# Optimization experiments

Measured on AMD Instinct MI355X. Metric: run time of the kernel, lower is better.

## Reference

```python
import jax, jax.numpy as jnp
import numpy as np

BANDWIDTH = 1.0


def setup_inputs() -> dict:
    key = jax.random.key(0)
    k1, k2 = jax.random.split(key)
    test_data = jax.random.normal(k1, (8192, 512), dtype=jnp.float32)
    train_data = jax.random.normal(k2, (16384, 512), dtype=jnp.float32)
    return {"test_data": test_data, "train_data": train_data}


def reference(test_data, train_data):
    # test_data: [N, D], train_data: [M, D]
    bw = jnp.asarray(BANDWIDTH, dtype=test_data.dtype)
    n_train, d = train_data.shape
    # (avoids materializing the [N, M, D] difference tensor)
    x2 = jnp.sum(test_data * test_data, axis=-1, keepdims=True)        # [N, 1]
    y2 = jnp.sum(train_data * train_data, axis=-1)[None, :]           # [1, M]
    xy = jnp.einsum('nd,md->nm', test_data, train_data)               # [N, M]
    sq_dist = jnp.maximum(x2 + y2 - 2.0 * xy, 0.0)                    # [N, M]
    log_exp = -0.5 * sq_dist / (bw * bw)
    # normalization constant z = 0.5*d*log(2*pi) + d*log(bw) + log(n)
    z = (0.5 * d * jnp.log(jnp.asarray(2.0 * np.pi, dtype=test_data.dtype))
         + d * jnp.log(bw)
         + jnp.log(jnp.asarray(float(n_train), dtype=test_data.dtype)))
    return jax.scipy.special.logsumexp(log_exp - z, axis=-1)          # [N]
```

## Files before the change

kernel.cpp:

```cpp
#include <hip/hip_runtime.h>

#define D 512
#define NTEST 8192
#define NTRAIN 16384
#define BN 128
#define BM 128
#define KB 128
#define NCHUNK 8
#define NPART (NCHUNK * 2)
#define CHUNK_M (NTRAIN / NCHUNK)
#define TILES (CHUNK_M / BM)
#define ZCONST 480.20058952863157f

typedef __attribute__((ext_vector_type(4))) int int4v;
typedef __attribute__((ext_vector_type(8))) int int8v;
typedef __attribute__((ext_vector_type(4))) float floatx4;

__device__ __forceinline__ void async_copy16(const void* g, void* l) {
  __builtin_amdgcn_global_load_lds(
      (const __attribute__((address_space(1))) unsigned int*)g,
      (__attribute__((address_space(3))) unsigned int*)l, 16, 0, 0);
}

__global__ __launch_bounds__(256) void prep_kernel(
    const float* __restrict__ test, const float* __restrict__ train,
    unsigned char* __restrict__ testq, unsigned char* __restrict__ trainq,
    float* __restrict__ x2, float* __restrict__ y2) {
  const int gw = (int)((blockIdx.x * blockDim.x + threadIdx.x) >> 6);
  const int lane = threadIdx.x & 63;
  const float* src;
  unsigned char* dst;
  float* sq;
  if (gw < NTEST) {
    src = test + (size_t)gw * D;
    dst = testq + (size_t)gw * D;
    sq = x2 + gw;
  } else {
    const int r = gw - NTEST;
    src = train + (size_t)r * D;
    dst = trainq + (size_t)r * D;
    sq = y2 + r;
  }
  const int kb = lane >> 4;
  const int q = (lane >> 2) & 3;
  const int h = (lane >> 1) & 1;
  const int hb = lane & 1;
  const int sbase = kb * 128 + q * 32 + h * 16 + hb * 8;
  const int dbase = kb * 128 + h * 64 + q * 16 + hb * 8;
  float4 v0 = *(const float4*)(src + sbase);
  float4 v1 = *(const float4*)(src + sbase + 4);
  float s = v0.x * v0.x + v0.y * v0.y + v0.z * v0.z + v0.w * v0.w +
            v1.x * v1.x + v1.y * v1.y + v1.z * v1.z + v1.w * v1.w;
  int w0 = __builtin_amdgcn_cvt_pk_fp8_f32(v0.x, v0.y, 0, false);
  w0 = __builtin_amdgcn_cvt_pk_fp8_f32(v0.z, v0.w, w0, true);
  int w1 = __builtin_amdgcn_cvt_pk_fp8_f32(v1.x, v1.y, 0, false);
  w1 = __builtin_amdgcn_cvt_pk_fp8_f32(v1.z, v1.w, w1, true);
  int2 pv;
  pv.x = w0;
  pv.y = w1;
  *(int2*)(dst + dbase) = pv;
#pragma unroll
  for (int off = 32; off >= 1; off >>= 1) s += __shfl_xor(s, off);
  if (lane == 0) *sq = s;
}

__global__ __launch_bounds__(256, 2) void fused_kernel(
    const unsigned char* __restrict__ A, const unsigned char* __restrict__ B,
    const float* __restrict__ y2, float* __restrict__ part_m,
    float* __restrict__ part_l) {
  __shared__ unsigned char sA0[BN * KB];
  __shared__ unsigned char sA1[BN * KB];
  __shared__ unsigned char sB0[BM * KB];
  __shared__ unsigned char sB1[BM * KB];
  const int tid = threadIdx.x;
  const int lane = tid & 63;
  const int w = tid >> 6;
  const int lm = lane & 15;
  const int lk = lane >> 4;
  const int rowbase = blockIdx.x * BN;
  const int chunk = blockIdx.y;
  const int wrow = (w >> 1) * 64;
  const int wcol = (w & 1) * 64;

  size_t aS[4], bS[4];
  int dO[4];
#pragma unroll
  for (int i = 0; i < 4; ++i) {
    const int o = tid * 16 + i * 4096;
    const int r = o >> 7;
    const int csw = (o >> 4) & 7;
    const int off = ((csw ^ (r & 7)) << 4);
    dO[i] = o;
    aS[i] = (size_t)(rowbase + r) * D + off;
    bS[i] = (size_t)r * D + off;
  }
  int aOffLo[4], aOffHi[4], bOffLo[4], bOffHi[4];
#pragma unroll
  for (int i = 0; i < 4; ++i) {
    const int arow = wrow + i * 16 + lm;
    aOffLo[i] = arow * KB + ((lk ^ (arow & 7)) << 4);
    aOffHi[i] = arow * KB + (((4 + lk) ^ (arow & 7)) << 4);
    const int brow = wcol + i * 16 + lm;
    bOffLo[i] = brow * KB + ((lk ^ (brow & 7)) << 4);
    bOffHi[i] = brow * KB + (((4 + lk) ^ (brow & 7)) << 4);
  }

  auto stage = [&](unsigned char* sa, unsigned char* sb, size_t bcolD,
                   int kb) {
#pragma unroll
    for (int i = 0; i < 4; ++i) {
      async_copy16(A + aS[i] + kb * 128, sa + dO[i]);
      async_copy16(B + bcolD + bS[i] + kb * 128, sb + dO[i]);
    }
  };

  floatx4 acc[4][4];
  auto compute = [&](const unsigned char* sa, const unsigned char* sb) {
    int8v af[4], bf[4];
#pragma unroll
    for (int rt = 0; rt < 4; ++rt) {
      int4v lo = *(const int4v*)&sa[aOffLo[rt]];
      int4v hi = *(const int4v*)&sa[aOffHi[rt]];
      af[rt] = __builtin_shufflevector(lo, hi, 0, 1, 2, 3, 4, 5, 6, 7);
    }
#pragma unroll
    for (int ct = 0; ct < 4; ++ct) {
      int4v lo = *(const int4v*)&sb[bOffLo[ct]];
      int4v hi = *(const int4v*)&sb[bOffHi[ct]];
      bf[ct] = __builtin_shufflevector(lo, hi, 0, 1, 2, 3, 4, 5, 6, 7);
    }
#pragma unroll
    for (int rt = 0; rt < 4; ++rt)
#pragma unroll
      for (int ct = 0; ct < 4; ++ct)
        acc[rt][ct] = __builtin_amdgcn_mfma_scale_f32_16x16x128_f8f6f4(
            af[rt], bf[ct], acc[rt][ct], 0, 0, 0, 127, 0, 127);
  };

  float run_m[16], run_l[16];
#pragma unroll
  for (int i = 0; i < 16; ++i) { run_m[i] = -1e30f; run_l[i] = 0.f; }

  stage(sA0, sB0, (size_t)(chunk * CHUNK_M) * D, 0);
  __syncthreads();

  for (int t = 0; t < TILES; ++t) {
    const int colbase = chunk * CHUNK_M + t * BM;
    const size_t bcolD = (size_t)colbase * D;
    float y2v[4];
#pragma unroll
    for (int ct = 0; ct < 4; ++ct)
      y2v[ct] = y2[colbase + wcol + ct * 16 + lm];

#pragma unroll
    for (int rt = 0; rt < 4; ++rt)
#pragma unroll
      for (int ct = 0; ct < 4; ++ct)
        acc[rt][ct] = floatx4{0.f, 0.f, 0.f, 0.f};

    stage(sA1, sB1, bcolD, 1);
    compute(sA0, sB0);
    __syncthreads();
    stage(sA0, sB0, bcolD, 2);
    compute(sA1, sB1);
    __syncthreads();
    stage(sA1, sB1, bcolD, 3);
    compute(sA0, sB0);
    __syncthreads();
    if (t + 1 < TILES) stage(sA0, sB0, bcolD + (size_t)BM * D, 0);
    compute(sA1, sB1);

#pragma unroll
    for (int rt = 0; rt < 4; ++rt) {
#pragma unroll
      for (int reg = 0; reg < 4; ++reg) {
        const int idx = rt * 4 + reg;
        const float v0 = fmaf(-0.5f, y2v[0], acc[rt][0][reg]);
        const float v1 = fmaf(-0.5f, y2v[1], acc[rt][1][reg]);
        const float v2 = fmaf(-0.5f, y2v[2], acc[rt][2][reg]);
        const float v3 = fmaf(-0.5f, y2v[3], acc[rt][3][reg]);
        const float tmax = fmaxf(fmaxf(v0, v1), fmaxf(v2, v3));
        const float nm = fmaxf(run_m[idx], tmax);
        const float alpha = __expf(run_m[idx] - nm);
        const float ps = __expf(v0 - nm) + __expf(v1 - nm) +
                         __expf(v2 - nm) + __expf(v3 - nm);
        run_l[idx] = fmaf(run_l[idx], alpha, ps);
        run_m[idx] = nm;
      }
    }
    __syncthreads();
  }

  const int slot = chunk * 2 + (w & 1);
#pragma unroll
  for (int rt = 0; rt < 4; ++rt) {
#pragma unroll
    for (int reg = 0; reg < 4; ++reg) {
      const int idx = rt * 4 + reg;
      float m = run_m[idx], l = run_l[idx];
#pragma unroll
      for (int off = 1; off < 16; off <<= 1) {
        const float om = __shfl_xor(m, off);
        const float ol = __shfl_xor(l, off);
        const float nm2 = fmaxf(m, om);
        l = l * __expf(m - nm2) + ol * __expf(om - nm2);
        m = nm2;
      }
      if (lm == 0) {
        const int grow = rowbase + wrow + rt * 16 + lk * 4 + reg;
        part_m[slot * NTEST + grow] = m;
        part_l[slot * NTEST + grow] = l;
      }
    }
  }
}

__global__ __launch_bounds__(256) void combine_kernel(
    const float* __restrict__ part_m, const float* __restrict__ part_l,
    const float* __restrict__ x2, float* __restrict__ out) {
  const int n = blockIdx.x * blockDim.x + threadIdx.x;
  if (n >= NTEST) return;
  float m[NPART];
  float mx = -1e30f;
#pragma unroll
  for (int c = 0; c < NPART; ++c) {
    m[c] = part_m[c * NTEST + n];
    mx = fmaxf(mx, m[c]);
  }
  float s = 0.f;
#pragma unroll
  for (int c = 0; c < NPART; ++c)
    s += part_l[c * NTEST + n] * __expf(m[c] - mx);
  out[n] = fmaf(-0.5f, x2[n], mx + __logf(s) - ZCONST);
}

extern "C" void kernel_launch(void* const* d_in, const int* in_sizes, int n_in,
                              void* d_out, int out_size, void* d_ws, size_t ws_size,
                              hipStream_t stream) {
  const float* test = (const float*)d_in[0];
  const float* train = (const float*)d_in[1];
  float* out = (float*)d_out;
  char* ws = (char*)d_ws;

  unsigned char* testq = (unsigned char*)ws;
  unsigned char* trainq = (unsigned char*)(ws + (size_t)NTEST * D);
  float* x2 = (float*)(ws + (size_t)(NTEST + NTRAIN) * D);
  float* y2 = x2 + NTEST;
  float* part_m = y2 + NTRAIN;
  float* part_l = part_m + NPART * NTEST;

  prep_kernel<<<(NTEST + NTRAIN) / 4, 256, 0, stream>>>(
      test, train, testq, trainq, x2, y2);
  fused_kernel<<<dim3(NTEST / BN, NCHUNK), 256, 0, stream>>>(
      testq, trainq, y2, part_m, part_l);
  combine_kernel<<<NTEST / 256, 256, 0, stream>>>(part_m, part_l, x2, out);
}
```

Before: 160.9 us.

## Replace double-buffered LDS pipeline with single buffer to allow three blocks per CU

```diff
diff --git a/kernel.cpp b/kernel.cpp
--- a/kernel.cpp
+++ b/kernel.cpp
@@ -64,14 +64,12 @@
   if (lane == 0) *sq = s;
 }
 
-__global__ __launch_bounds__(256, 2) void fused_kernel(
+__global__ __launch_bounds__(256, 3) void fused_kernel(
     const unsigned char* __restrict__ A, const unsigned char* __restrict__ B,
     const float* __restrict__ y2, float* __restrict__ part_m,
     float* __restrict__ part_l) {
-  __shared__ unsigned char sA0[BN * KB];
-  __shared__ unsigned char sA1[BN * KB];
-  __shared__ unsigned char sB0[BM * KB];
-  __shared__ unsigned char sB1[BM * KB];
+  __shared__ unsigned char sA[BN * KB];
+  __shared__ unsigned char sB[BM * KB];
   const int tid = threadIdx.x;
   const int lane = tid & 63;
   const int w = tid >> 6;
@@ -105,28 +103,27 @@
     bOffHi[i] = brow * KB + (((4 + lk) ^ (brow & 7)) << 4);
   }
 
-  auto stage = [&](unsigned char* sa, unsigned char* sb, size_t bcolD,
-                   int kb) {
+  auto stage = [&](size_t bcolD, int kb) {
 #pragma unroll
     for (int i = 0; i < 4; ++i) {
-      async_copy16(A + aS[i] + kb * 128, sa + dO[i]);
-      async_copy16(B + bcolD + bS[i] + kb * 128, sb + dO[i]);
+      async_copy16(A + aS[i] + kb * 128, sA + dO[i]);
+      async_copy16(B + bcolD + bS[i] + kb * 128, sB + dO[i]);
     }
   };
 
   floatx4 acc[4][4];
-  auto compute = [&](const unsigned char* sa, const unsigned char* sb) {
+  auto compute = [&]() {
     int8v af[4], bf[4];
 #pragma unroll
     for (int rt = 0; rt < 4; ++rt) {
-      int4v lo = *(const int4v*)&sa[aOffLo[rt]];
-      int4v hi = *(const int4v*)&sa[aOffHi[rt]];
+      int4v lo = *(const int4v*)&sA[aOffLo[rt]];
+      int4v hi = *(const int4v*)&sA[aOffHi[rt]];
       af[rt] = __builtin_shufflevector(lo, hi, 0, 1, 2, 3, 4, 5, 6, 7);
     }
 #pragma unroll
     for (int ct = 0; ct < 4; ++ct) {
-      int4v lo = *(const int4v*)&sb[bOffLo[ct]];
-      int4v hi = *(const int4v*)&sb[bOffHi[ct]];
+      int4v lo = *(const int4v*)&sB[bOffLo[ct]];
+      int4v hi = *(const int4v*)&sB[bOffHi[ct]];
       bf[ct] = __builtin_shufflevector(lo, hi, 0, 1, 2, 3, 4, 5, 6, 7);
     }
 #pragma unroll
@@ -141,9 +138,6 @@
 #pragma unroll
   for (int i = 0; i < 16; ++i) { run_m[i] = -1e30f; run_l[i] = 0.f; }
 
-  stage(sA0, sB0, (size_t)(chunk * CHUNK_M) * D, 0);
-  __syncthreads();
-
   for (int t = 0; t < TILES; ++t) {
     const int colbase = chunk * CHUNK_M + t * BM;
     const size_t bcolD = (size_t)colbase * D;
@@ -158,17 +152,12 @@
       for (int ct = 0; ct < 4; ++ct)
         acc[rt][ct] = floatx4{0.f, 0.f, 0.f, 0.f};
 
-    stage(sA1, sB1, bcolD, 1);
-    compute(sA0, sB0);
-    __syncthreads();
-    stage(sA0, sB0, bcolD, 2);
-    compute(sA1, sB1);
-    __syncthreads();
-    stage(sA1, sB1, bcolD, 3);
-    compute(sA0, sB0);
-    __syncthreads();
-    if (t + 1 < TILES) stage(sA0, sB0, bcolD + (size_t)BM * D, 0);
-    compute(sA1, sB1);
+    for (int kb = 0; kb < D / KB; ++kb) {
+      __syncthreads();
+      stage(bcolD, kb);
+      __syncthreads();
+      compute();
+    }
 
 #pragma unroll
     for (int rt = 0; rt < 4; ++rt) {
@@ -188,7 +177,6 @@
         run_m[idx] = nm;
       }
     }
-    __syncthreads();
   }
 
   const int slot = chunk * 2 + (w & 1);
```

After: 251.9 us. 56.5% more time.
